# Performance work log

Measured on AMD Instinct MI355X. Metric: run time of the kernel, lower is better.

Reference implementation:

```python
import jax, jax.numpy as jnp
import numpy as np

B, LENS_T, LENS_S, DIM, HEADS, RANK = 64, 64, 256, 768, 12, 64
HEAD_DIM = DIM // HEADS


def setup_inputs() -> dict:
    key = jax.random.key(0)
    ks = jax.random.split(key, 12)
    s = 0.02
    return {
        "x0": jax.random.normal(ks[0], (B, LENS_T + LENS_S, DIM), jnp.float32),
        "x1": jax.random.normal(ks[1], (B, LENS_T + LENS_S, DIM), jnp.float32),
        "ln1_w": jnp.ones((DIM,), jnp.float32),
        "ln1_b": jnp.zeros((DIM,), jnp.float32),
        "ln2_w": jnp.ones((DIM,), jnp.float32),
        "ln2_b": jnp.zeros((DIM,), jnp.float32),
        "wq": jax.random.normal(ks[2], (DIM, DIM), jnp.float32) * s,
        "wk": jax.random.normal(ks[3], (DIM, DIM), jnp.float32) * s,
        "wv": jax.random.normal(ks[4], (DIM, DIM), jnp.float32) * s,
        "wo": jax.random.normal(ks[5], (DIM, DIM), jnp.float32) * s,
        "lora_down": jax.random.normal(ks[6], (DIM, RANK), jnp.float32) * s,
        "lora_up": jax.random.normal(ks[7], (RANK, DIM), jnp.float32) * s,
        "mlp_down": jax.random.normal(ks[8], (DIM, RANK), jnp.float32) * s,
        "mlp_up": jax.random.normal(ks[9], (RANK, DIM), jnp.float32) * s,
        "lens_t": LENS_T,
    }


def _layernorm(x, w, b, eps=1e-5):
    mu = x.mean(-1, keepdims=True)
    var = ((x - mu) ** 2).mean(-1, keepdims=True)
    return (x - mu) * jax.lax.rsqrt(var + eps) * w + b


def _cross_attn(q_in, kv_in, wq, wk, wv, wo):
    Bq, Nq, _ = q_in.shape
    Nk = kv_in.shape[1]
    q = (q_in @ wq).reshape(Bq, Nq, HEADS, HEAD_DIM)
    k = (kv_in @ wk).reshape(Bq, Nk, HEADS, HEAD_DIM)
    v = (kv_in @ wv).reshape(Bq, Nk, HEADS, HEAD_DIM)
    scale = HEAD_DIM ** -0.5
    logits = jnp.einsum("bqhd,bkhd->bhqk", q, k) * scale
    attn = jax.nn.softmax(logits, axis=-1)  # [B,H,Nq,Nk]
    out = jnp.einsum("bhqk,bkhd->bqhd", attn, v).reshape(Bq, Nq, DIM)
    return out @ wo, attn


def _lora(x, down, up):
    return jax.nn.gelu(x @ down) @ up


def _fusion(token_T, token_S, attn):
    # affinity: sum over heads, transpose -> [B, Ns, Nt]
    affinity = attn.sum(axis=1).transpose(0, 2, 1)
    aff_max = affinity.max(axis=1, keepdims=True)  # max over search tokens
    mask = (affinity == aff_max).astype(token_S.dtype)
    numerator = jnp.exp(affinity - 12.0) * mask
    denominator = 1.0 + numerator.sum(axis=-1, keepdims=True)
    token_S = token_S / denominator + jnp.einsum(
        "bst,btd->bsd", numerator / denominator, token_T
    )
    return jnp.concatenate([token_T, token_S], axis=1)


def reference(x0, x1, ln1_w, ln1_b, ln2_w, ln2_b, wq, wk, wv, wo,
              lora_down, lora_up, mlp_down, mlp_up, lens_t):
    z_rgb, x_rgb = x0[:, :lens_t], x0[:, lens_t:]
    z_dte, x_dte = x1[:, :lens_t], x1[:, lens_t:]

    ln1 = lambda t: _layernorm(t, ln1_w, ln1_b)
    crs_rgb, attn_rgb = _cross_attn(ln1(z_rgb), ln1(x_dte), wq, wk, wv, wo)
    crs_dte, attn_dte = _cross_attn(ln1(z_dte), ln1(x_rgb), wq, wk, wv, wo)

    fuse_zrgb = z_rgb + crs_rgb + _lora(ln1(z_dte), lora_down, lora_up)
    fuse_zdte = z_dte + crs_dte + _lora(ln1(z_rgb), lora_down, lora_up)

    y0 = _fusion(fuse_zrgb, x_rgb, attn_rgb)
    y1 = _fusion(fuse_zdte, x_dte, attn_dte)

    ln2 = lambda t: _layernorm(t, ln2_w, ln2_b)
    y0 = y0 + _lora(ln2(y0), mlp_down, mlp_up)
    y1 = y1 + _lora(ln2(y1), mlp_down, mlp_up)
    return jnp.stack([y0, y1], axis=0)  # [2, B, N, D]
```

## Files before the change

### kernel.cpp

```cpp
#include <hip/hip_runtime.h>


typedef __bf16 bf8_t __attribute__((ext_vector_type(8)));
typedef float f4_t __attribute__((ext_vector_type(4)));
typedef unsigned short u16;
typedef unsigned int u32;
typedef unsigned long long u64;
typedef unsigned short us4_t __attribute__((ext_vector_type(4)));
typedef unsigned short us8_t __attribute__((ext_vector_type(8)));

__device__ __forceinline__ float bf2f(u16 h) {
    return __uint_as_float(((unsigned int)h) << 16);
}
__device__ __forceinline__ u16 f2bf(float f) {
    unsigned int u = __float_as_uint(f);
    u += 0x7fffu + ((u >> 16) & 1u);
    return (u16)(u >> 16);
}
__device__ __forceinline__ float gelu_tanh(float x) {
    float t = tanhf(0.7978845608028654f * (x + 0.044715f * x * x * x));
    return 0.5f * x * (1.0f + t);
}
__device__ __forceinline__ void load_lds16(const void* g, void* l) {
    __builtin_amdgcn_global_load_lds(
        (const __attribute__((address_space(1))) unsigned int*)g,
        (__attribute__((address_space(3))) unsigned int*)l, 16, 0, 0);
}

struct TPack {
    const float* s0; const float* s1; const float* s2; const float* s3;
    u16* d0; u16* d1; u16* d2; u16* d3;
};
__global__ __launch_bounds__(256) void transpose_big(TPack p) {
    int which = blockIdx.y;
    const float* src = which == 0 ? p.s0 : which == 1 ? p.s1 : which == 2 ? p.s2 : p.s3;
    u16* dst = which == 0 ? p.d0 : which == 1 ? p.d1 : which == 2 ? p.d2 : p.d3;
    int idx = blockIdx.x * 256 + threadIdx.x;
    int c = idx / 768, r = idx - c * 768;
    u16 v = f2bf(src[(size_t)r * 768 + c]);
    if (which == 3) dst[(size_t)c * 832 + r] = v;
    else dst[idx] = v;
}
__global__ __launch_bounds__(256) void transpose_small(TPack p) {
    int which = blockIdx.y;
    const float* src = which == 0 ? p.s0 : which == 1 ? p.s1 : which == 2 ? p.s2 : p.s3;
    u16* dst = which == 0 ? p.d0 : which == 1 ? p.d1 : which == 2 ? p.d2 : p.d3;
    int R = (which & 1) ? 64 : 768;
    int C = (which & 1) ? 768 : 64;
    int idx = blockIdx.x * 256 + threadIdx.x;
    int c = idx / R, r = idx - c * R;
    u16 v = f2bf(src[(size_t)r * C + c]);
    if (which == 1) dst[(size_t)c * 832 + r] = v;
    else dst[idx] = v;
}

__global__ __launch_bounds__(256) void ln1_kernel(
    const float* __restrict__ x0, const float* __restrict__ x1,
    const float* __restrict__ w, const float* __restrict__ b,
    u16* __restrict__ lnZ, u16* __restrict__ lnX) {
    int rid = blockIdx.x * 4 + (threadIdx.x >> 6);
    int lane = threadIdx.x & 63;
    int s = rid / 20480;
    int r2 = rid - s * 20480;
    const float* srcBase = (s == 0) ? x0 : x1;
    const float* src; u16* dst;
    if (r2 < 4096) {
        int bb = r2 >> 6, t = r2 & 63;
        src = srcBase + ((size_t)(bb * 320 + t)) * 768;
        dst = lnZ + ((size_t)(s * 4096 + r2)) * 768;
    } else {
        int rx = r2 - 4096;
        int bb = rx >> 8, sx = rx & 255;
        src = srcBase + ((size_t)(bb * 320 + 64 + sx)) * 768;
        dst = lnX + ((size_t)(s * 16384 + rx)) * 768;
    }
    f4_t v[3];
    float s1 = 0.f, s2 = 0.f;
    #pragma unroll
    for (int jj = 0; jj < 3; jj++) {
        v[jj] = *reinterpret_cast<const f4_t*>(src + (lane + 64 * jj) * 4);
        #pragma unroll
        for (int e = 0; e < 4; e++) { s1 += v[jj][e]; s2 += v[jj][e] * v[jj][e]; }
    }
    #pragma unroll
    for (int o = 1; o < 64; o <<= 1) { s1 += __shfl_xor(s1, o); s2 += __shfl_xor(s2, o); }
    float mean = s1 * (1.0f / 768.0f);
    float var = s2 * (1.0f / 768.0f) - mean * mean;
    float rstd = rsqrtf(var + 1e-5f);
    #pragma unroll
    for (int jj = 0; jj < 3; jj++) {
        int c0 = (lane + 64 * jj) * 4;
        f4_t wv = *reinterpret_cast<const f4_t*>(w + c0);
        f4_t bv = *reinterpret_cast<const f4_t*>(b + c0);
        us4_t o4;
        #pragma unroll
        for (int e = 0; e < 4; e++)
            o4[e] = f2bf((v[jj][e] - mean) * rstd * wv[e] + bv[e]);
        *reinterpret_cast<us4_t*>(dst + c0) = o4;
    }
}

enum { EPI_BF16 = 0, EPI_RESID_Z = 1, EPI_GELU64 = 2 };

template <int BM, int BN, int WR, int WC, int EPI, int KT>
__device__ __forceinline__ void gemm_core(
    u16* shA, u16* shB,
    const u16* __restrict__ A, const u16* __restrict__ Bt,
    int M, int N, int ldc, int xb, int bid,
    float* __restrict__ Cf, u16* __restrict__ Cbf,
    const float* __restrict__ resid0, const float* __restrict__ resid1) {
    constexpr int THREADS = WR * WC * 64;
    constexpr int NW = THREADS / 64;
    constexpr int BK = 64;

    const int tid = threadIdx.x;
    const int lane = tid & 63;
    const int w = tid >> 6;
    const int wr = w / WC, wc = w % WC;
    const int r = lane & 15, g = lane >> 4;
    const int gx = N / BN;
    const int panels = (M / BM) >> 3;
    int xcd = bid & 7, local = bid >> 3;
    const int bcol = (local % gx) * BN;
    const int brow = (xcd * panels + local / gx) * BM;

    const int srow = lane >> 3;
    const int scol = (lane & 7) ^ srow;
    const int rsw = r & 7;
    const int csw0 = (g ^ rsw) * 8;
    const int csw1 = ((g + 4) ^ rsw) * 8;
    int aoff[4], boff[4];
    #pragma unroll
    for (int m = 0; m < 4; m++) aoff[m] = (wr * 64 + m * 16 + r) * 64;
    #pragma unroll
    for (int n = 0; n < 4; n++) boff[n] = (wc * 64 + n * 16 + r) * 64;

    f4_t acc[4][4];
    f4_t zero = {0.f, 0.f, 0.f, 0.f};
    #pragma unroll
    for (int m = 0; m < 4; m++)
        #pragma unroll
        for (int n = 0; n < 4; n++) acc[m][n] = zero;

    for (int k0 = 0; k0 < KT; k0 += BK) {
        #pragma unroll
        for (int c = 0; c < BM / 8 / NW; c++) {
            int chunk = w + c * NW;
            int row = chunk * 8 + srow;
            load_lds16(A + (size_t)(brow + row) * KT + k0 + scol * 8, shA + chunk * 512);
        }
        #pragma unroll
        for (int c = 0; c < BN / 8 / NW; c++) {
            int chunk = w + c * NW;
            int row = chunk * 8 + srow;
            load_lds16(Bt + (size_t)(bcol + row) * KT + k0 + scol * 8, shB + chunk * 512);
        }
        __syncthreads();
        {
            bf8_t af[4], bfr[4];
            #pragma unroll
            for (int m = 0; m < 4; m++)
                af[m] = *reinterpret_cast<const bf8_t*>(&shA[aoff[m] + csw0]);
            #pragma unroll
            for (int n = 0; n < 4; n++)
                bfr[n] = *reinterpret_cast<const bf8_t*>(&shB[boff[n] + csw0]);
            #pragma unroll
            for (int m = 0; m < 4; m++)
                #pragma unroll
                for (int n = 0; n < 4; n++)
                    acc[m][n] = __builtin_amdgcn_mfma_f32_16x16x32_bf16(af[m], bfr[n], acc[m][n], 0, 0, 0);
            #pragma unroll
            for (int m = 0; m < 4; m++)
                af[m] = *reinterpret_cast<const bf8_t*>(&shA[aoff[m] + csw1]);
            #pragma unroll
            for (int n = 0; n < 4; n++)
                bfr[n] = *reinterpret_cast<const bf8_t*>(&shB[boff[n] + csw1]);
            #pragma unroll
            for (int m = 0; m < 4; m++)
                #pragma unroll
                for (int n = 0; n < 4; n++)
                    acc[m][n] = __builtin_amdgcn_mfma_f32_16x16x32_bf16(af[m], bfr[n], acc[m][n], 0, 0, 0);
        }
        __syncthreads();
    }

    #pragma unroll
    for (int m = 0; m < 4; m++) {
        #pragma unroll
        for (int n = 0; n < 4; n++) {
            int col = bcol + wc * 64 + n * 16 + r;
            #pragma unroll
            for (int i = 0; i < 4; i++) {
                int row = brow + wr * 64 + m * 16 + g * 4 + i;
                int orow = row ^ xb;
                float val = acc[m][n][i];
                if constexpr (EPI == EPI_BF16) {
                    Cbf[(size_t)orow * ldc + col] = f2bf(val);
                } else if constexpr (EPI == EPI_RESID_Z) {
                    int s = orow >> 12, bb = (orow >> 6) & 63, t = orow & 63;
                    const float* rp = (s != 0) ? resid1 : resid0;
                    float rs = rp[((size_t)bb * 320 + t) * 768 + col];
                    Cf[(size_t)orow * 768 + col] = val + rs;
                } else if constexpr (EPI == EPI_GELU64) {
                    if (col < 64)
                        Cbf[(size_t)orow * ldc + col] = f2bf(gelu_tanh(val));
                }
            }
        }
    }
}

struct ProjArgs {
    const u16* lnZ; const u16* lnX; const u16* wtq; const u16* wtkv;
    u16* qb; u16* kvb;
};
__global__ __launch_bounds__(256, 1) void gemm_proj(ProjArgs a) {
    __shared__ alignas(16) u16 SH[16384];
    int bid = blockIdx.x;
    if (bid < 384) {
        gemm_core<128, 128, 2, 2, EPI_BF16, 768>(
            SH, SH + 8192, a.lnZ, a.wtq, 8192, 768, 768, 0, bid,
            nullptr, a.qb, nullptr, nullptr);
    } else {
        gemm_core<128, 128, 2, 2, EPI_BF16, 768>(
            SH, SH + 8192, a.lnX, a.wtkv, 32768, 1536, 1536, 16384, bid - 384,
            nullptr, a.kvb, nullptr, nullptr);
    }
}

struct AttnArgs {
    const u16* q; const u16* kv; u16* aoh; u16* paff;
    const u16* lnZ; const u16* dT; u16* aohL;
};
__global__ __launch_bounds__(256, 2) void attn_mfma(AttnArgs a) {
    __shared__ alignas(16) u16 Ks[256][72];
    __shared__ alignas(16) u16 Vt[64][264];
    int bid0 = blockIdx.x;
    if (bid0 < 64) {
        u16* SH = &Ks[0][0];
        gemm_core<128, 128, 2, 2, EPI_GELU64, 768>(
            SH, SH + 8192, a.lnZ, a.dT, 8192, 128, 832, 4096, bid0,
            nullptr, a.aohL, nullptr, nullptr);
        return;
    }
    int bid = bid0 - 64;
    const u16* q = a.q;
    const u16* kv = a.kv;
    u16* aoh = a.aoh;
    u16* paff = a.paff;
    int s = bid / 768;
    int rem = bid - s * 768;
    int b = rem / 12, h = rem - (rem / 12) * 12;
    int tid = threadIdx.x, lane = tid & 63, w = tid >> 6;
    int r = lane & 15, g = lane >> 4;

    size_t kvbase = ((size_t)(s * 16384 + b * 256)) * 1536 + h * 64;

    const u16* qrow = q + ((size_t)(s * 4096 + b * 64 + w * 16 + r)) * 768 + h * 64 + g * 8;
    bf8_t qf0 = *reinterpret_cast<const bf8_t*>(qrow);
    bf8_t qf1 = *reinterpret_cast<const bf8_t*>(qrow + 32);

    #pragma unroll
    for (int i = 0; i < 8; i++) {
        int c = tid + 256 * i;
        int row = c >> 3, kc = (c & 7) * 8;
        *reinterpret_cast<bf8_t*>(&Ks[row][kc]) =
            *reinterpret_cast<const bf8_t*>(kv + kvbase + (size_t)row * 1536 + kc);
    }
    u32* vt32 = reinterpret_cast<u32*>(&Vt[0][0]);
    #pragma unroll
    for (int i = 0; i < 4; i++) {
        int c = tid + 256 * i;
        int kp = c >> 3, d0 = (c & 7) * 8;
        const u16* vr = kv + kvbase + 768 + (size_t)(2 * kp) * 1536 + d0;
        us8_t va = *reinterpret_cast<const us8_t*>(vr);
        us8_t vb = *reinterpret_cast<const us8_t*>(vr + 1536);
        #pragma unroll
        for (int j = 0; j < 8; j++)
            vt32[(d0 + j) * 132 + kp] = (u32)va[j] | ((u32)vb[j] << 16);
    }
    __syncthreads();

    f4_t acc[16];
    f4_t zero = {0.f, 0.f, 0.f, 0.f};
    #pragma unroll
    for (int n = 0; n < 16; n++) acc[n] = zero;
    #pragma unroll
    for (int n = 0; n < 16; n++) {
        bf8_t b0 = *reinterpret_cast<const bf8_t*>(&Ks[n * 16 + r][g * 8]);
        acc[n] = __builtin_amdgcn_mfma_f32_16x16x32_bf16(qf0, b0, acc[n], 0, 0, 0);
        bf8_t b1 = *reinterpret_cast<const bf8_t*>(&Ks[n * 16 + r][32 + g * 8]);
        acc[n] = __builtin_amdgcn_mfma_f32_16x16x32_bf16(qf1, b1, acc[n], 0, 0, 0);
    }

    float mx[4] = {-1e30f, -1e30f, -1e30f, -1e30f};
    #pragma unroll
    for (int n = 0; n < 16; n++)
        #pragma unroll
        for (int i = 0; i < 4; i++) {
            acc[n][i] *= 0.125f;
            mx[i] = fmaxf(mx[i], acc[n][i]);
        }
    #pragma unroll
    for (int i = 0; i < 4; i++) {
        mx[i] = fmaxf(mx[i], __shfl_xor(mx[i], 1));
        mx[i] = fmaxf(mx[i], __shfl_xor(mx[i], 2));
        mx[i] = fmaxf(mx[i], __shfl_xor(mx[i], 4));
        mx[i] = fmaxf(mx[i], __shfl_xor(mx[i], 8));
    }
    float sm[4] = {0.f, 0.f, 0.f, 0.f};
    #pragma unroll
    for (int n = 0; n < 16; n++)
        #pragma unroll
        for (int i = 0; i < 4; i++) {
            float e = __expf(acc[n][i] - mx[i]);
            acc[n][i] = e;
            sm[i] += e;
        }
    #pragma unroll
    for (int i = 0; i < 4; i++) {
        sm[i] += __shfl_xor(sm[i], 1);
        sm[i] += __shfl_xor(sm[i], 2);
        sm[i] += __shfl_xor(sm[i], 4);
        sm[i] += __shfl_xor(sm[i], 8);
    }
    float inv[4];
    #pragma unroll
    for (int i = 0; i < 4; i++) inv[i] = 1.0f / sm[i];

    __syncthreads();

    u16* Pw = &Ks[w * 64][0];
    u16* pout = paff + ((size_t)bid * 64 + w * 16) * 256;
    #pragma unroll
    for (int n = 0; n < 16; n++) {
        int kcol = n * 16 + r;
        #pragma unroll
        for (int i = 0; i < 4; i++) {
            u16 pb = f2bf(acc[n][i] * inv[i]);
            Pw[(g * 4 + i) * 264 + kcol] = pb;
            pout[(g * 4 + i) * 256 + kcol] = pb;
        }
    }

    f4_t acc2[4];
    #pragma unroll
    for (int n = 0; n < 4; n++) acc2[n] = zero;
    #pragma unroll
    for (int k2 = 0; k2 < 8; k2++) {
        bf8_t pa = *reinterpret_cast<const bf8_t*>(&Pw[r * 264 + k2 * 32 + g * 8]);
        #pragma unroll
        for (int n2 = 0; n2 < 4; n2++) {
            bf8_t vbf = *reinterpret_cast<const bf8_t*>(&Vt[n2 * 16 + r][k2 * 32 + g * 8]);
            acc2[n2] = __builtin_amdgcn_mfma_f32_16x16x32_bf16(pa, vbf, acc2[n2], 0, 0, 0);
        }
    }
    u16* op = aoh + ((size_t)(s * 4096 + b * 64 + w * 16 + g * 4)) * 832 + h * 64;
    #pragma unroll
    for (int n2 = 0; n2 < 4; n2++)
        #pragma unroll
        for (int i = 0; i < 4; i++)
            op[(size_t)i * 832 + n2 * 16 + r] = f2bf(acc2[n2][i]);
}

__device__ __forceinline__ void prep2_body(
    int idx, const u16* __restrict__ paff, float* __restrict__ aff,
    float* __restrict__ den, u64* __restrict__ winners, float* red) {
    int sb = idx & 127, qc = idx >> 7;
    int t = threadIdx.x, lane = t & 63, w = t >> 6;
    int q0 = qc * 16;
    float a[16];
    #pragma unroll
    for (int j = 0; j < 16; j++) a[j] = 0.f;
    size_t base = ((size_t)sb * 12 * 64 + q0) * 256 + t;
    for (int h = 0; h < 12; h++) {
        size_t hb = base + (size_t)h * 64 * 256;
        #pragma unroll
        for (int j = 0; j < 16; j++) a[j] += bf2f(paff[hb + j * 256]);
    }
    float m[16];
    #pragma unroll
    for (int j = 0; j < 16; j++) {
        float v = a[j];
        #pragma unroll
        for (int o = 1; o < 64; o <<= 1) v = fmaxf(v, __shfl_xor(v, o));
        m[j] = v;
    }
    if (lane == 0) {
        #pragma unroll
        for (int j = 0; j < 16; j++) red[j * 4 + w] = m[j];
    }
    __syncthreads();
    float dsum = 0.f;
    u64 wmask = 0;
    float nu[16];
    #pragma unroll
    for (int j = 0; j < 16; j++) {
        float cm = fmaxf(fmaxf(red[j * 4 + 0], red[j * 4 + 1]),
                         fmaxf(red[j * 4 + 2], red[j * 4 + 3]));
        nu[j] = (a[j] == cm) ? __expf(a[j] - 12.0f) : 0.f;
        if (nu[j] != 0.f) wmask |= (u64)1 << (q0 + j);
        dsum += nu[j];
    }
    if (dsum != 0.f) atomicAdd(&den[sb * 256 + t], dsum);
    if (wmask) atomicOr(&winners[(size_t)sb * 256 + t], wmask);
    float* ap = aff + ((size_t)sb * 256 + t) * 64 + q0;
    #pragma unroll
    for (int j = 0; j < 16; j++) ap[j] = nu[j];
}

struct PostArgs {
    const u16* aoh; const u16* wtoU; float* zbuf;
    const float* x0; const float* x1;
    const u16* paff; float* aff; float* den; u64* winners;
};
__global__ __launch_bounds__(256, 1) void gemm_post(PostArgs a) {
    __shared__ alignas(16) u16 SH[16384];
    int bid = blockIdx.x;
    if (bid < 384) {
        gemm_core<128, 128, 2, 2, EPI_RESID_Z, 832>(
            SH, SH + 8192, a.aoh, a.wtoU, 8192, 768, 768, 0, bid,
            a.zbuf, nullptr, a.x0, a.x1);
    } else {
        prep2_body(bid - 384, a.paff, a.aff, a.den, a.winners, (float*)SH);
    }
}

__global__ __launch_bounds__(256, 2) void fusion_ln2_mlp(
    const float* __restrict__ x0, const float* __restrict__ x1,
    const float* __restrict__ zbuf, const float* __restrict__ aff,
    const float* __restrict__ den, const u64* __restrict__ winners,
    float* __restrict__ out, const float* __restrict__ w2,
    const float* __restrict__ b2, const u16* __restrict__ mdT,
    const u16* __restrict__ muT) {
    __shared__ alignas(16) u16 A[16][776];
    __shared__ alignas(16) u16 Hs[16][72];
    int tid = threadIdx.x, lane = tid & 63, w = tid >> 6;
    int r = lane & 15, g = lane >> 4;
    int rbase = blockIdx.x * 16;

    const float* srcp[4];
    float scale[4];
    u64 masks[4];
    int sbx[4], sxx[4], sss[4];
    #pragma unroll
    for (int rr = 0; rr < 4; rr++) {
        int rid = rbase + w * 4 + rr;
        int s = rid / 20480;
        int r2 = rid - s * 20480;
        int b = r2 / 320, n = r2 - (r2 / 320) * 320;
        sss[rr] = s; sbx[rr] = b;
        if (n < 64) {
            srcp[rr] = zbuf + ((size_t)(s * 4096 + b * 64 + n)) * 768;
            scale[rr] = 1.0f;
            masks[rr] = 0;
            sxx[rr] = 0;
        } else {
            int sx = n - 64;
            int sb = s * 64 + b;
            srcp[rr] = ((s == 0) ? x0 : x1) + ((size_t)(b * 320 + n)) * 768;
            scale[rr] = 1.0f / (1.0f + den[sb * 256 + sx]);
            masks[rr] = winners[(size_t)sb * 256 + sx];
            sxx[rr] = sx;
        }
    }
    f4_t p[4][3];
    #pragma unroll
    for (int rr = 0; rr < 4; rr++)
        #pragma unroll
        for (int cc = 0; cc < 3; cc++)
            p[rr][cc] = *reinterpret_cast<const f4_t*>(srcp[rr] + cc * 256 + lane * 4);
    u64 many = (masks[0] & (masks[0] - 1)) | (masks[1] & (masks[1] - 1)) |
               (masks[2] & (masks[2] - 1)) | (masks[3] & (masks[3] - 1));
    u64 anyw = masks[0] | masks[1] | masks[2] | masks[3];
    if (many == 0) {
        if (anyw) {
            int wt[4];
            float wnu[4];
            #pragma unroll
            for (int rr = 0; rr < 4; rr++)
                wt[rr] = masks[rr] ? (int)__builtin_ctzll(masks[rr]) : 0;
            #pragma unroll
            for (int rr = 0; rr < 4; rr++) {
                size_t sb = (size_t)(sss[rr] * 64 + sbx[rr]);
                wnu[rr] = aff[(sb * 256 + sxx[rr]) * 64 + wt[rr]];
            }
            f4_t zv[4][3];
            #pragma unroll
            for (int rr = 0; rr < 4; rr++) {
                const float* zr = zbuf + ((size_t)(sss[rr] * 4096 + sbx[rr] * 64 + wt[rr])) * 768;
                #pragma unroll
                for (int cc = 0; cc < 3; cc++)
                    zv[rr][cc] = *reinterpret_cast<const f4_t*>(zr + cc * 256 + lane * 4);
            }
            #pragma unroll
            for (int rr = 0; rr < 4; rr++) {
                float wgt = masks[rr] ? wnu[rr] * scale[rr] : 0.f;
                #pragma unroll
                for (int cc = 0; cc < 3; cc++)
                    p[rr][cc] = p[rr][cc] * scale[rr] + zv[rr][cc] * wgt;
            }
        }
    } else {
        #pragma unroll
        for (int rr = 0; rr < 4; rr++) {
            #pragma unroll
            for (int cc = 0; cc < 3; cc++) p[rr][cc] *= scale[rr];
            u64 mask = masks[rr];
            while (mask) {
                int t = (int)__builtin_ctzll(mask);
                mask &= mask - 1;
                int sb = sss[rr] * 64 + sbx[rr];
                float wgt = aff[((size_t)sb * 256 + sxx[rr]) * 64 + t] * scale[rr];
                const float* zr = zbuf + ((size_t)(sss[rr] * 4096 + sbx[rr] * 64 + t)) * 768;
                #pragma unroll
                for (int cc = 0; cc < 3; cc++)
                    p[rr][cc] += *reinterpret_cast<const f4_t*>(zr + cc * 256 + lane * 4) * wgt;
            }
        }
    }
    f4_t wv[3], bv[3];
    #pragma unroll
    for (int cc = 0; cc < 3; cc++) {
        wv[cc] = *reinterpret_cast<const f4_t*>(w2 + cc * 256 + lane * 4);
        bv[cc] = *reinterpret_cast<const f4_t*>(b2 + cc * 256 + lane * 4);
    }
    #pragma unroll
    for (int rr = 0; rr < 4; rr++) {
        float a1 = 0.f, a2 = 0.f;
        #pragma unroll
        for (int cc = 0; cc < 3; cc++)
            #pragma unroll
            for (int e = 0; e < 4; e++) { a1 += p[rr][cc][e]; a2 += p[rr][cc][e] * p[rr][cc][e]; }
        #pragma unroll
        for (int o = 1; o < 64; o <<= 1) { a1 += __shfl_xor(a1, o); a2 += __shfl_xor(a2, o); }
        float mean = a1 * (1.0f / 768.0f);
        float var = a2 * (1.0f / 768.0f) - mean * mean;
        float rstd = rsqrtf(var + 1e-5f);
        int row = w * 4 + rr;
        #pragma unroll
        for (int cc = 0; cc < 3; cc++) {
            int c0 = cc * 256 + lane * 4;
            us4_t o4;
            #pragma unroll
            for (int e = 0; e < 4; e++)
                o4[e] = f2bf((p[rr][cc][e] - mean) * rstd * wv[cc][e] + bv[cc][e]);
            *reinterpret_cast<us4_t*>(&A[row][c0]) = o4;
        }
    }
    __syncthreads();

    f4_t zero = {0.f, 0.f, 0.f, 0.f};
    f4_t hacc = zero;
    const u16* mrow = mdT + (size_t)(w * 16 + r) * 768 + g * 8;
    #pragma unroll
    for (int k0 = 0; k0 < 768; k0 += 32) {
        bf8_t af = *reinterpret_cast<const bf8_t*>(&A[r][k0 + g * 8]);
        bf8_t bf = *reinterpret_cast<const bf8_t*>(mrow + k0);
        hacc = __builtin_amdgcn_mfma_f32_16x16x32_bf16(af, bf, hacc, 0, 0, 0);
    }
    #pragma unroll
    for (int i = 0; i < 4; i++)
        Hs[g * 4 + i][w * 16 + r] = f2bf(gelu_tanh(hacc[i]));
    __syncthreads();

    bf8_t a0 = *reinterpret_cast<const bf8_t*>(&Hs[r][g * 8]);
    bf8_t a1 = *reinterpret_cast<const bf8_t*>(&Hs[r][32 + g * 8]);
    #pragma unroll
    for (int nn = 0; nn < 12; nn++) {
        int col = w * 192 + nn * 16 + r;
        bf8_t b0 = *reinterpret_cast<const bf8_t*>(muT + (size_t)col * 64 + g * 8);
        bf8_t b1 = *reinterpret_cast<const bf8_t*>(muT + (size_t)col * 64 + 32 + g * 8);
        f4_t c = __builtin_amdgcn_mfma_f32_16x16x32_bf16(a1, b1, zero, 0, 0, 0);
        c = __builtin_amdgcn_mfma_f32_16x16x32_bf16(a0, b0, c, 0, 0, 0);
        #pragma unroll
        for (int i = 0; i < 4; i++)
            A[g * 4 + i][col] = f2bf(c[i]);
    }
    __syncthreads();

    #pragma unroll
    for (int rr = 0; rr < 4; rr++) {
        int row = w * 4 + rr;
        size_t orow = (size_t)(rbase + row) * 768;
        #pragma unroll
        for (int cc = 0; cc < 3; cc++) {
            int c0 = cc * 256 + lane * 4;
            us4_t c4 = *reinterpret_cast<const us4_t*>(&A[row][c0]);
            f4_t o = p[rr][cc];
            #pragma unroll
            for (int e = 0; e < 4; e++) o[e] += bf2f(c4[e]);
            *reinterpret_cast<f4_t*>(out + orow + c0) = o;
        }
    }
}

extern "C" void kernel_launch(void* const* d_in, const int* in_sizes, int n_in,
                              void* d_out, int out_size, void* d_ws, size_t ws_size,
                              hipStream_t stream) {
    (void)in_sizes; (void)n_in; (void)out_size;
    const float* x0 = (const float*)d_in[0];
    const float* x1 = (const float*)d_in[1];
    const float* ln1w = (const float*)d_in[2];
    const float* ln1b = (const float*)d_in[3];
    const float* ln2w = (const float*)d_in[4];
    const float* ln2b = (const float*)d_in[5];
    const float* wq = (const float*)d_in[6];
    const float* wk = (const float*)d_in[7];
    const float* wv = (const float*)d_in[8];
    const float* wo = (const float*)d_in[9];
    const float* lora_down = (const float*)d_in[10];
    const float* lora_up = (const float*)d_in[11];
    const float* mlp_down = (const float*)d_in[12];
    const float* mlp_up = (const float*)d_in[13];
    float* out = (float*)d_out;

    char* ws = (char*)d_ws;
    size_t off = 0;
    auto alloc = [&](size_t bytes) -> char* {
        char* p = ws + off;
        off = (off + bytes + 255) & ~(size_t)255;
        return p;
    };
    u16* wtq  = (u16*)alloc(768 * 768 * 2);
    u16* wtkv = (u16*)alloc((size_t)1536 * 768 * 2);
    u16* wtoU = (u16*)alloc((size_t)768 * 832 * 2);
    u16* dT  = (u16*)alloc((size_t)128 * 768 * 2);
    u16* mdT = (u16*)alloc(768 * 64 * 2);
    u16* muT = (u16*)alloc(768 * 64 * 2);
    u16* lnZ = (u16*)alloc((size_t)2 * 4096 * 768 * 2);
    u16* lnX = (u16*)alloc((size_t)2 * 16384 * 768 * 2);
    u16* qb  = (u16*)alloc((size_t)2 * 4096 * 768 * 2);
    u16* kvb = (u16*)alloc((size_t)2 * 16384 * 1536 * 2);
    u16* aoh = (u16*)alloc((size_t)2 * 4096 * 832 * 2);
    float* aff = (float*)alloc((size_t)2 * 64 * 256 * 64 * 4);
    float* den = (float*)alloc((size_t)2 * 64 * 256 * 4);
    u64* winners = (u64*)alloc((size_t)2 * 64 * 256 * 8);
    u16* paff = lnX;
    float* zbuf = (float*)kvb;
    if (ws_size < off) return;

    hipMemsetAsync(dT, 0, (size_t)128 * 768 * 2, stream);
    TPack big = {wq, wk, wv, wo, wtq, wtkv, wtkv + (size_t)768 * 768, wtoU};
    transpose_big<<<dim3(2304, 4), 256, 0, stream>>>(big);
    TPack small = {lora_down, lora_up, mlp_down, mlp_up, dT, wtoU + 768, mdT, muT};
    transpose_small<<<dim3(192, 4), 256, 0, stream>>>(small);
    hipMemsetAsync(den, 0, (size_t)2 * 64 * 256 * 4, stream);
    hipMemsetAsync(winners, 0, (size_t)2 * 64 * 256 * 8, stream);
    ln1_kernel<<<10240, 256, 0, stream>>>(x0, x1, ln1w, ln1b, lnZ, lnX);
    ProjArgs pa = {lnZ, lnX, wtq, wtkv, qb, kvb};
    gemm_proj<<<3456, 256, 0, stream>>>(pa);
    AttnArgs aa = {qb, kvb, aoh, paff, lnZ, dT, aoh + 768};
    attn_mfma<<<1600, 256, 0, stream>>>(aa);
    PostArgs po = {aoh, wtoU, zbuf, x0, x1, paff, aff, den, winners};
    gemm_post<<<896, 256, 0, stream>>>(po);
    fusion_ln2_mlp<<<2560, 256, 0, stream>>>(
        x0, x1, zbuf, aff, den, winners, out, ln2w, ln2b, mdT, muT);
}
```

Measured before the change: 340.7 us.

## Use 512-thread blocks in fusion/LN2/MLP kernel with two rows per wave

```diff
diff --git a/kernel.cpp b/kernel.cpp
--- a/kernel.cpp
+++ b/kernel.cpp
@@ -426,7 +426,7 @@
     }
 }
 
-__global__ __launch_bounds__(256, 2) void fusion_ln2_mlp(
+__global__ __launch_bounds__(512, 8) void fusion_ln2_mlp(
     const float* __restrict__ x0, const float* __restrict__ x1,
     const float* __restrict__ zbuf, const float* __restrict__ aff,
     const float* __restrict__ den, const u64* __restrict__ winners,
@@ -439,94 +439,43 @@
     int r = lane & 15, g = lane >> 4;
     int rbase = blockIdx.x * 16;
 
-    const float* srcp[4];
-    float scale[4];
-    u64 masks[4];
-    int sbx[4], sxx[4], sss[4];
-    #pragma unroll
-    for (int rr = 0; rr < 4; rr++) {
-        int rid = rbase + w * 4 + rr;
+    f4_t p[2][3];
+    #pragma unroll
+    for (int rr = 0; rr < 2; rr++) {
+        int row = w * 2 + rr;
+        int rid = rbase + row;
         int s = rid / 20480;
         int r2 = rid - s * 20480;
         int b = r2 / 320, n = r2 - (r2 / 320) * 320;
-        sss[rr] = s; sbx[rr] = b;
+        const float* srcp;
+        float scale;
+        u64 mask;
+        const float* zrbase = zbuf + ((size_t)(s * 4096 + b * 64)) * 768;
+        const float* affbase = nullptr;
         if (n < 64) {
-            srcp[rr] = zbuf + ((size_t)(s * 4096 + b * 64 + n)) * 768;
-            scale[rr] = 1.0f;
-            masks[rr] = 0;
-            sxx[rr] = 0;
+            srcp = zrbase + (size_t)n * 768;
+            scale = 1.0f;
+            mask = 0;
         } else {
             int sx = n - 64;
             int sb = s * 64 + b;
-            srcp[rr] = ((s == 0) ? x0 : x1) + ((size_t)(b * 320 + n)) * 768;
-            scale[rr] = 1.0f / (1.0f + den[sb * 256 + sx]);
-            masks[rr] = winners[(size_t)sb * 256 + sx];
-            sxx[rr] = sx;
-        }
-    }
-    f4_t p[4][3];
-    #pragma unroll
-    for (int rr = 0; rr < 4; rr++)
+            srcp = ((s == 0) ? x0 : x1) + ((size_t)(b * 320 + n)) * 768;
+            scale = 1.0f / (1.0f + den[sb * 256 + sx]);
+            mask = winners[(size_t)sb * 256 + sx];
+            affbase = aff + ((size_t)sb * 256 + sx) * 64;
+        }
         #pragma unroll
         for (int cc = 0; cc < 3; cc++)
-            p[rr][cc] = *reinterpret_cast<const f4_t*>(srcp[rr] + cc * 256 + lane * 4);
-    u64 many = (masks[0] & (masks[0] - 1)) | (masks[1] & (masks[1] - 1)) |
-               (masks[2] & (masks[2] - 1)) | (masks[3] & (masks[3] - 1));
-    u64 anyw = masks[0] | masks[1] | masks[2] | masks[3];
-    if (many == 0) {
-        if (anyw) {
-            int wt[4];
-            float wnu[4];
-            #pragma unroll
-            for (int rr = 0; rr < 4; rr++)
-                wt[rr] = masks[rr] ? (int)__builtin_ctzll(masks[rr]) : 0;
-            #pragma unroll
-            for (int rr = 0; rr < 4; rr++) {
-                size_t sb = (size_t)(sss[rr] * 64 + sbx[rr]);
-                wnu[rr] = aff[(sb * 256 + sxx[rr]) * 64 + wt[rr]];
-            }
-            f4_t zv[4][3];
-            #pragma unroll
-            for (int rr = 0; rr < 4; rr++) {
-                const float* zr = zbuf + ((size_t)(sss[rr] * 4096 + sbx[rr] * 64 + wt[rr])) * 768;
-                #pragma unroll
-                for (int cc = 0; cc < 3; cc++)
-                    zv[rr][cc] = *reinterpret_cast<const f4_t*>(zr + cc * 256 + lane * 4);
-            }
-            #pragma unroll
-            for (int rr = 0; rr < 4; rr++) {
-                float wgt = masks[rr] ? wnu[rr] * scale[rr] : 0.f;
-                #pragma unroll
-                for (int cc = 0; cc < 3; cc++)
-                    p[rr][cc] = p[rr][cc] * scale[rr] + zv[rr][cc] * wgt;
-            }
-        }
-    } else {
-        #pragma unroll
-        for (int rr = 0; rr < 4; rr++) {
-            #pragma unroll
-            for (int cc = 0; cc < 3; cc++) p[rr][cc] *= scale[rr];
-            u64 mask = masks[rr];
-            while (mask) {
-                int t = (int)__builtin_ctzll(mask);
-                mask &= mask - 1;
-                int sb = sss[rr] * 64 + sbx[rr];
-                float wgt = aff[((size_t)sb * 256 + sxx[rr]) * 64 + t] * scale[rr];
-                const float* zr = zbuf + ((size_t)(sss[rr] * 4096 + sbx[rr] * 64 + t)) * 768;
-                #pragma unroll
-                for (int cc = 0; cc < 3; cc++)
-                    p[rr][cc] += *reinterpret_cast<const f4_t*>(zr + cc * 256 + lane * 4) * wgt;
-            }
-        }
-    }
-    f4_t wv[3], bv[3];
-    #pragma unroll
-    for (int cc = 0; cc < 3; cc++) {
-        wv[cc] = *reinterpret_cast<const f4_t*>(w2 + cc * 256 + lane * 4);
-        bv[cc] = *reinterpret_cast<const f4_t*>(b2 + cc * 256 + lane * 4);
-    }
-    #pragma unroll
-    for (int rr = 0; rr < 4; rr++) {
+            p[rr][cc] = *reinterpret_cast<const f4_t*>(srcp + cc * 256 + lane * 4) * scale;
+        while (mask) {
+            int t = (int)__builtin_ctzll(mask);
+            mask &= mask - 1;
+            float wgt = affbase[t] * scale;
+            const float* zr = zrbase + (size_t)t * 768;
+            #pragma unroll
+            for (int cc = 0; cc < 3; cc++)
+                p[rr][cc] += *reinterpret_cast<const f4_t*>(zr + cc * 256 + lane * 4) * wgt;
+        }
         float a1 = 0.f, a2 = 0.f;
         #pragma unroll
         for (int cc = 0; cc < 3; cc++)
@@ -537,38 +486,41 @@
         float mean = a1 * (1.0f / 768.0f);
         float var = a2 * (1.0f / 768.0f) - mean * mean;
         float rstd = rsqrtf(var + 1e-5f);
-        int row = w * 4 + rr;
         #pragma unroll
         for (int cc = 0; cc < 3; cc++) {
             int c0 = cc * 256 + lane * 4;
+            f4_t wv = *reinterpret_cast<const f4_t*>(w2 + c0);
+            f4_t bv = *reinterpret_cast<const f4_t*>(b2 + c0);
             us4_t o4;
             #pragma unroll
             for (int e = 0; e < 4; e++)
-                o4[e] = f2bf((p[rr][cc][e] - mean) * rstd * wv[cc][e] + bv[cc][e]);
+                o4[e] = f2bf((p[rr][cc][e] - mean) * rstd * wv[e] + bv[e]);
             *reinterpret_cast<us4_t*>(&A[row][c0]) = o4;
         }
     }
     __syncthreads();
 
     f4_t zero = {0.f, 0.f, 0.f, 0.f};
-    f4_t hacc = zero;
-    const u16* mrow = mdT + (size_t)(w * 16 + r) * 768 + g * 8;
-    #pragma unroll
-    for (int k0 = 0; k0 < 768; k0 += 32) {
-        bf8_t af = *reinterpret_cast<const bf8_t*>(&A[r][k0 + g * 8]);
-        bf8_t bf = *reinterpret_cast<const bf8_t*>(mrow + k0);
-        hacc = __builtin_amdgcn_mfma_f32_16x16x32_bf16(af, bf, hacc, 0, 0, 0);
-    }
-    #pragma unroll
-    for (int i = 0; i < 4; i++)
-        Hs[g * 4 + i][w * 16 + r] = f2bf(gelu_tanh(hacc[i]));
+    if (w < 4) {
+        f4_t hacc = zero;
+        const u16* mrow = mdT + (size_t)(w * 16 + r) * 768 + g * 8;
+        #pragma unroll
+        for (int k0 = 0; k0 < 768; k0 += 32) {
+            bf8_t af = *reinterpret_cast<const bf8_t*>(&A[r][k0 + g * 8]);
+            bf8_t bf = *reinterpret_cast<const bf8_t*>(mrow + k0);
+            hacc = __builtin_amdgcn_mfma_f32_16x16x32_bf16(af, bf, hacc, 0, 0, 0);
+        }
+        #pragma unroll
+        for (int i = 0; i < 4; i++)
+            Hs[g * 4 + i][w * 16 + r] = f2bf(gelu_tanh(hacc[i]));
+    }
     __syncthreads();
 
     bf8_t a0 = *reinterpret_cast<const bf8_t*>(&Hs[r][g * 8]);
     bf8_t a1 = *reinterpret_cast<const bf8_t*>(&Hs[r][32 + g * 8]);
     #pragma unroll
-    for (int nn = 0; nn < 12; nn++) {
-        int col = w * 192 + nn * 16 + r;
+    for (int nn = 0; nn < 6; nn++) {
+        int col = w * 96 + nn * 16 + r;
         bf8_t b0 = *reinterpret_cast<const bf8_t*>(muT + (size_t)col * 64 + g * 8);
         bf8_t b1 = *reinterpret_cast<const bf8_t*>(muT + (size_t)col * 64 + 32 + g * 8);
         f4_t c = __builtin_amdgcn_mfma_f32_16x16x32_bf16(a1, b1, zero, 0, 0, 0);
@@ -580,8 +532,8 @@
     __syncthreads();
 
     #pragma unroll
-    for (int rr = 0; rr < 4; rr++) {
-        int row = w * 4 + rr;
+    for (int rr = 0; rr < 2; rr++) {
+        int row = w * 2 + rr;
         size_t orow = (size_t)(rbase + row) * 768;
         #pragma unroll
         for (int cc = 0; cc < 3; cc++) {
@@ -654,6 +606,6 @@
     attn_mfma<<<1600, 256, 0, stream>>>(aa);
     PostArgs po = {aoh, wtoU, zbuf, x0, x1, paff, aff, den, winners};
     gemm_post<<<896, 256, 0, stream>>>(po);
-    fusion_ln2_mlp<<<2560, 256, 0, stream>>>(
+    fusion_ln2_mlp<<<2560, 512, 0, stream>>>(
         x0, x1, zbuf, aff, den, winners, out, ln2w, ln2b, mdT, muT);
 }
```

Result: no change. 345.2 us (+1.3%).
